# Kernel tuning notes

Measured on AMD Instinct MI355X. Metric: run time of the kernel, lower is better.

Reference implementation:

```python
import jax, jax.numpy as jnp
import numpy as np
from jax import lax

NUM_CLASSES = 8          # channel dim of pred_out -> alphabet of argmax values
NUM_TARGET_LABELS = 8    # fill_max of target_mask -> alphabet of target labels
BIG = 2 ** 30            # sentinel for min-propagation connected components


def connected_components(mask):
    """4-connected components per image. mask: [B,H,W] bool.
    Returns (labels, idx): labels int32, 0 = background; a component's label is
    (min flat index in component) + 1, so labels are unique across the batch.
    Uses min-label propagation to convergence (jit-compatible while_loop)."""
    B, H, W = mask.shape
    idx = jnp.arange(B * H * W, dtype=jnp.int32).reshape(B, H, W) + 1
    lab0 = jnp.where(mask, idx, 0)

    def step(lab):
        l = jnp.where(mask, lab, BIG)
        p = jnp.pad(l, ((0, 0), (1, 1), (1, 1)), constant_values=BIG)
        nb = jnp.minimum(jnp.minimum(p[:, :-2, 1:-1], p[:, 2:, 1:-1]),
                         jnp.minimum(p[:, 1:-1, :-2], p[:, 1:-1, 2:]))
        return jnp.where(mask, jnp.minimum(l, nb), 0)

    def cond(c):
        return jnp.logical_not(c[1])

    def body(c):
        lab, _ = c
        new = step(lab)
        return new, jnp.all(new == lab)

    lab, _ = lax.while_loop(cond, body, (lab0, jnp.array(False)))
    return lab, idx


def bce_dice(pred, target, eps=1e-7, smooth=1.0):
    """BCEDiceLoss: mean binary cross-entropy (pred in [0,1]) + soft dice loss."""
    p = jnp.clip(pred, eps, 1.0 - eps)
    bce = -jnp.mean(target * jnp.log(p) + (1.0 - target) * jnp.log(1.0 - p))
    inter = jnp.sum(pred * target)
    dice = 1.0 - (2.0 * inter + smooth) / (jnp.sum(pred) + jnp.sum(target) + smooth)
    return bce + dice


def build_placeholder(pred_masks):
    """Faithful vectorized form of the per-class / per-component torch loops.
    For each present class v != 0, for each component c != 0 the original does
    placeholder += c_mask * c + last_i  (note: last_i is added GLOBALLY -- we
    replicate that), i.e. placeholder += cc_labels + n_comp * last_i, and
    last_i += len(unique(cc)) = n_comp + (1 if background present)."""
    placeholder = jnp.zeros(pred_masks.shape, dtype=jnp.float32)
    last_i = jnp.int32(1)
    for v in range(1, NUM_CLASSES):  # fixed alphabet of argmax values
        m = pred_masks == v
        present = jnp.any(m)
        lab, idx = connected_components(m)
        n_comp = jnp.sum((lab == idx) & m).astype(jnp.int32)  # one rep per comp
        has_bg = jnp.any(jnp.logical_not(m)).astype(jnp.int32)
        contrib = lab.astype(jnp.float32) + n_comp.astype(jnp.float32) * last_i.astype(jnp.float32)
        placeholder = placeholder + jnp.where(present, contrib, 0.0)
        last_i = last_i + jnp.where(present, n_comp + has_bg, 0)
    return placeholder


def reference(pred_out, target_mask):
    pred_masks = jnp.argmax(pred_out, axis=1)  # [B,H,W]
    # background term
    res = bce_dice((pred_out[:, 0:1] * (pred_masks[:, None] == 0)).astype(jnp.float32),
                   (target_mask == 0).astype(jnp.float32))
    placeholder = build_placeholder(pred_masks)
    # per-target-instance median matching (loop over fixed label alphabet,
    # guarded by presence, since torch loops over the data-dependent unique set)
    for t in range(1, NUM_TARGET_LABELS):
        tm = (target_mask == t)[:, 0]  # [B,H,W]
        n = jnp.sum(tm).astype(jnp.int32)
        present = n > 0
        vals = jnp.sort(jnp.where(tm, placeholder, jnp.inf).ravel())
        med = vals[jnp.maximum(n - 1, 0) // 2]  # torch lower median
        full_med = (placeholder == med).astype(jnp.float32)
        res = res + jnp.where(present, bce_dice(full_med, tm.astype(jnp.float32)), 0.0)
    n_uniq = jnp.sum(jnp.stack([jnp.any(target_mask == t)
                                for t in range(NUM_TARGET_LABELS)])).astype(jnp.float32)
    return res / (n_uniq + 1.0)


def setup_inputs():
    key = jax.random.key(0)
    k1, k2 = jax.random.split(key)
    pred_out = jax.random.uniform(k1, (4, NUM_CLASSES, 512, 512), dtype=jnp.float32)
    target_mask = jax.random.randint(k2, (4, 1, 512, 512), 0, NUM_TARGET_LABELS,
                                     dtype=jnp.int32)
    return {"pred_out": pred_out, "target_mask": target_mask}
```

## Files before the change

kernel.cpp:

```cpp
#include <hip/hip_runtime.h>
#include <math.h>


#define HWMASK (262144 - 1)
#define AL(p) __hip_atomic_load((p), __ATOMIC_RELAXED, __HIP_MEMORY_SCOPE_AGENT)
#define AS(p, v) __hip_atomic_store((p), (v), __ATOMIC_RELAXED, __HIP_MEMORY_SCOPE_AGENT)
#define REL(p, v) __hip_atomic_store((p), (v), __ATOMIC_RELEASE, __HIP_MEMORY_SCOPE_AGENT)
#define ARRIVE(p) __hip_atomic_fetch_add((p), 1u, __ATOMIC_RELAXED, __HIP_MEMORY_SCOPE_AGENT)

static __device__ __forceinline__ int ufind(int* p, int x) {
  while (true) {
    int px = p[x];
    if (px == x) return x;
    int g = p[px];
    if (g == px) return px;
    p[x] = g;
    x = g;
  }
}

static __device__ __forceinline__ int unite(int* p, int a, int b) {
  while (true) {
    a = ufind(p, a); b = ufind(p, b);
    if (a == b) return 0;
    if (a < b) { int old = atomicCAS(&p[b], b, a); if (old == b) return 1; b = old; }
    else       { int old = atomicCAS(&p[a], a, b); if (old == a) return 1; a = old; }
  }
}

__global__ __launch_bounds__(256) void k_argmax(
    const float* __restrict__ pred, const int* __restrict__ tgt,
    int* __restrict__ parent, unsigned char* __restrict__ pk,
    unsigned* __restrict__ stats, unsigned* __restrict__ pcnt,
    double* __restrict__ pdbl, int N) {
  __shared__ unsigned hc[32], ht[32], hA, hB;
  __shared__ double dred[12];
  int tid = threadIdx.x, bid = blockIdx.x;
  if (bid == 0) {
    uint4* z = (uint4*)stats;
    for (int j = tid; j < 6144; j += 256) z[j] = make_uint4(0u, 0u, 0u, 0u);
  }
  if (tid < 32) { hc[tid] = 0; ht[tid] = 0; }
  if (tid == 0) { hA = 0; hB = 0; }
  __syncthreads();
  int wb = (tid >> 6) << 3;
  int n4 = N >> 2, gsz = gridDim.x * blockDim.x;
  double aL = 0.0, aI = 0.0, aP = 0.0;
  unsigned nA = 0, nB = 0;
  for (int i4 = bid * blockDim.x + tid; i4 < n4; i4 += gsz) {
    int i = i4 << 2;
    int b = i >> 18, hw = i & HWMASK;
    const float* pp = pred + ((size_t)b << 21) + hw;
    float4 v[8];
#pragma unroll
    for (int ch = 0; ch < 8; ++ch) v[ch] = *(const float4*)(pp + ((size_t)ch << 18));
    int4 tv = *(const int4*)(tgt + i);
    int tarr[4] = {tv.x & 7, tv.y & 7, tv.z & 7, tv.w & 7};
    unsigned char pkb[4];
#pragma unroll
    for (int j = 0; j < 4; ++j) {
      float p0 = ((const float*)&v[0])[j];
      float best = p0; int c = 0;
#pragma unroll
      for (int ch = 1; ch < 8; ++ch) {
        float x = ((const float*)&v[ch])[j];
        if (x > best) { best = x; c = ch; }
      }
      int t = tarr[j];
      pkb[j] = (unsigned char)(c | (t << 3));
      atomicAdd(&hc[wb + c], 1u);
      atomicAdd(&ht[wb + t], 1u);
      if (c == 0) {
        float pc = fminf(fmaxf(p0, 1e-7f), 1.0f - 1e-7f);
        if (t == 0) { aL += (double)logf(pc); aI += (double)p0; }
        else        { aL += (double)logf(1.0f - pc); }
        aP += (double)p0;
      } else { if (t == 0) nA++; else nB++; }
    }
    *(int4*)(parent + i) = make_int4(i, i + 1, i + 2, i + 3);
    *(uchar4*)(pk + i) = make_uchar4(pkb[0], pkb[1], pkb[2], pkb[3]);
  }
  if (nA) atomicAdd(&hA, nA);
  if (nB) atomicAdd(&hB, nB);
#pragma unroll
  for (int o = 32; o > 0; o >>= 1) {
    aL += __shfl_down(aL, o); aI += __shfl_down(aI, o); aP += __shfl_down(aP, o);
  }
  int wid = tid >> 6, lane = tid & 63;
  if (lane == 0) { dred[wid] = aL; dred[4 + wid] = aI; dred[8 + wid] = aP; }
  __syncthreads();
  if (tid < 8) {
    pcnt[bid * 20 + tid]     = hc[tid] + hc[8 + tid] + hc[16 + tid] + hc[24 + tid];
    pcnt[bid * 20 + 8 + tid] = ht[tid] + ht[8 + tid] + ht[16 + tid] + ht[24 + tid];
  }
  if (tid == 0) {
    pcnt[bid * 20 + 16] = hA; pcnt[bid * 20 + 17] = hB;
    pcnt[bid * 20 + 18] = 0u; pcnt[bid * 20 + 19] = 0u;
    pdbl[bid * 3 + 0] = dred[0] + dred[1] + dred[2] + dred[3];
    pdbl[bid * 3 + 1] = dred[4] + dred[5] + dred[6] + dred[7];
    pdbl[bid * 3 + 2] = dred[8] + dred[9] + dred[10] + dred[11];
  }
}

__global__ __launch_bounds__(256) void k_merge(
    const unsigned char* __restrict__ pk, int* __restrict__ parent,
    unsigned* __restrict__ stats, const unsigned* __restrict__ pcnt,
    unsigned* __restrict__ mcnt, int N, int nbam) {
  __shared__ unsigned lcnt[8], tot[26];
  __shared__ int lastM;
  int tid = threadIdx.x, bid = blockIdx.x;
  if (tid < 8) lcnt[tid] = 0;
  __syncthreads();
  int n4 = N >> 2, gsz = gridDim.x * blockDim.x;
  for (int i4 = bid * blockDim.x + tid; i4 < n4; i4 += gsz) {
    int i = i4 << 2;
    int hw = i & HWMASK;
    uchar4 a = *(const uchar4*)(pk + i);
    unsigned char ca[4] = {(unsigned char)(a.x & 7), (unsigned char)(a.y & 7),
                           (unsigned char)(a.z & 7), (unsigned char)(a.w & 7)};
    if (ca[0] && ca[0] == ca[1] && unite(parent, i,     i + 1)) atomicAdd(&lcnt[ca[0]], 1u);
    if (ca[1] && ca[1] == ca[2] && unite(parent, i + 1, i + 2)) atomicAdd(&lcnt[ca[1]], 1u);
    if (ca[2] && ca[2] == ca[3] && unite(parent, i + 2, i + 3)) atomicAdd(&lcnt[ca[2]], 1u);
    if ((hw & 511) < 508) {
      unsigned char nx = pk[i + 4] & 7;
      if (ca[3] && ca[3] == nx && unite(parent, i + 3, i + 4)) atomicAdd(&lcnt[ca[3]], 1u);
    }
    if ((hw >> 9) < 511) {
      uchar4 d = *(const uchar4*)(pk + i + 512);
      unsigned char da[4] = {(unsigned char)(d.x & 7), (unsigned char)(d.y & 7),
                             (unsigned char)(d.z & 7), (unsigned char)(d.w & 7)};
#pragma unroll
      for (int j = 0; j < 4; ++j)
        if (ca[j] && ca[j] == da[j] && unite(parent, i + j, i + j + 512))
          atomicAdd(&lcnt[ca[j]], 1u);
    }
  }
  __syncthreads();
  if (tid < 8) AS(&mcnt[bid * 8 + tid], lcnt[tid]);
  __syncthreads();
  if (tid == 0) lastM = (ARRIVE(&stats[76]) == gridDim.x - 1) ? 1 : 0;
  __syncthreads();
  if (!lastM) return;
  unsigned S[26];
#pragma unroll
  for (int k = 0; k < 26; ++k) S[k] = 0u;
  for (int b = tid; b < nbam; b += 256) {
    const unsigned* p = pcnt + b * 20;
#pragma unroll
    for (int k = 0; k < 18; ++k) S[k] += p[k];
#pragma unroll
    for (int k = 0; k < 8; ++k) S[18 + k] += AL(&mcnt[b * 8 + k]);
  }
  if (tid < 26) tot[tid] = 0u;
  __syncthreads();
#pragma unroll
  for (int k = 0; k < 26; ++k) {
    unsigned s = S[k];
#pragma unroll
    for (int o = 32; o > 0; o >>= 1) s += __shfl_down(s, o);
    if ((tid & 63) == 0 && s) atomicAdd(&tot[k], s);
  }
  __syncthreads();
  if (tid != 0) return;
  float prodf[8]; int last_i = 1; unsigned pb = 0;
  for (int v = 1; v < 8; ++v) {
    unsigned cntv = tot[v];
    unsigned ncv = cntv - tot[18 + v];
    prodf[v] = 0.0f;
    if (cntv) {
      prodf[v] = __fmul_rn((float)ncv, (float)last_i);
      pb |= 1u << v;
      last_i += (int)ncv + ((cntv < (unsigned)N) ? 1 : 0);
    }
    stats[24 + v] = __float_as_uint(prodf[v]);
  }
  float ph0 = 0.0f;
  for (int v = 1; v < 8; ++v) if (pb & (1u << v)) ph0 = __fadd_rn(ph0, prodf[v]);
  unsigned ab = 0;
  for (int t = 0; t < 8; ++t) stats[8 + t] = tot[8 + t];
  for (int t = 1; t < 8; ++t) {
    unsigned n = tot[8 + t];
    stats[48 + t] = n ? ((n - 1) >> 1) : 0u;
    if (n) ab |= 1u << t;
  }
  stats[32] = pb; stats[33] = ab;
  stats[34] = tot[16]; stats[35] = tot[17];
  unsigned pbits = __float_as_uint(ph0);
  stats[36] = pbits;
  unsigned c;
  if (pbits == 0) c = 64u;
  else {
    int e = (int)(pbits >> 23) - 127;
    int sh = 43 - e;
    if (sh <= 0) c = 64u;
    else if (sh >= 31) c = 0x7FFFFFFFu;
    else c = (1u << sh) + 64u;
  }
  int bl = 32 - __clz((int)c);
  stats[37] = (bl > 8) ? (unsigned)(bl - 8) : 0u;
}

static __device__ void scan_select(unsigned* __restrict__ stats,
                                   const unsigned* __restrict__ ghist,
                                   unsigned abm, int s_cur, unsigned* lh) {
  int tid = threadIdx.x;
  for (int t = 1; t < 8; ++t) {
    if (!(abm >> t & 1u)) continue;
    int k = (int)AL(&stats[48 + t]);
    unsigned cnt = 0;
#pragma unroll
    for (int r = 0; r < 8; ++r)
      cnt += AL(&ghist[r * 2048 + (t << 8) + tid]);
    lh[tid] = cnt;
    __syncthreads();
    for (int o = 1; o < 256; o <<= 1) {
      unsigned v = (tid >= o) ? lh[tid - o] : 0u;
      __syncthreads();
      lh[tid] += v;
      __syncthreads();
    }
    unsigned incl = lh[tid], excl = incl - cnt;
    if ((unsigned)k >= excl && (unsigned)k < incl) {
      atomicOr(&stats[40 + t], ((unsigned)tid) << s_cur);
      AS(&stats[48 + t], (unsigned)(k - (int)excl));
    }
    __syncthreads();
  }
}

static __device__ void finalize_loss(unsigned* __restrict__ stats,
                                     const double* __restrict__ pdbl,
                                     float* __restrict__ out, int N, int nbam,
                                     unsigned ab, double* dred) {
  int tid = threadIdx.x;
  double vL = 0.0, vI = 0.0, vP = 0.0;
  for (int b = tid; b < nbam; b += 256) {
    vL += pdbl[b * 3]; vI += pdbl[b * 3 + 1]; vP += pdbl[b * 3 + 2];
  }
#pragma unroll
  for (int o = 32; o > 0; o >>= 1) {
    vL += __shfl_down(vL, o); vI += __shfl_down(vI, o); vP += __shfl_down(vP, o);
  }
  int wid = tid >> 6, lane = tid & 63;
  if (lane == 0) { dred[wid] = vL; dred[4 + wid] = vI; dred[8 + wid] = vP; }
  __syncthreads();
  if (tid != 0) return;
  vL = dred[0] + dred[1] + dred[2] + dred[3];
  vI = dred[4] + dred[5] + dred[6] + dred[7];
  vP = dred[8] + dred[9] + dred[10] + dred[11];
  double Nd = (double)N;
  const float e32 = 1e-7f;
  const float c1 = 1.0f - e32;
  const float omc1 = 1.0f - c1;
  double lp1 = log((double)c1);
  double lp0 = log((double)e32);
  double l01 = log((double)omc1);
  double l00 = lp1;
  double L = vL + (double)stats[34] * lp0 + (double)stats[35] * l00;
  double res = -L / Nd;
  res += 1.0 - (2.0 * vI + 1.0) / (vP + (double)stats[8] + 1.0);
  for (int t = 1; t < 8; ++t) {
    if (ab >> t & 1u) {
      double a = (double)AL(&stats[56 + t]);
      double f = (double)AL(&stats[64 + t]);
      double n = (double)stats[8 + t];
      double bce = -(a * lp1 + (n - a) * lp0 + (f - a) * l01 + (Nd - n - f + a) * l00) / Nd;
      double dice = 1.0 - (2.0 * a + 1.0) / (f + n + 1.0);
      res += bce + dice;
    }
  }
  int nu = 0;
  for (int t = 0; t < 8; ++t) nu += (stats[8 + t] > 0) ? 1 : 0;
  out[0] = (float)(res / ((double)nu + 1.0));
}

__global__ __launch_bounds__(256, 4) void k_phase2(
    const unsigned char* __restrict__ pk, const int* __restrict__ parent,
    unsigned* __restrict__ stats, unsigned* __restrict__ ghist,
    const double* __restrict__ pdbl, float* __restrict__ out, int N, int nbam) {
  __shared__ unsigned lh[2176];
  __shared__ float sprod[8];
  __shared__ unsigned sw[32];
  __shared__ double dred[12];
  int tid = threadIdx.x;
  int lane = tid & 63;
  if (tid < 8) sprod[tid] = __uint_as_float(stats[24 + tid]);
  if (tid == 0) { sw[0] = stats[32]; sw[1] = stats[33]; sw[2] = stats[36]; sw[3] = stats[37]; }
  for (int j = tid; j < 2176; j += 256) lh[j] = 0u;
  __syncthreads();
  unsigned pb = sw[0], ab = sw[1], ph0 = sw[2];
  int s1 = (int)sw[3];
  unsigned rep = (blockIdx.x & 7) * 2048u;
  int n4 = N >> 2;
  unsigned kk[4];
  unsigned char tv8[4], binv[4];
  int i4 = blockIdx.x * blockDim.x + tid;
  if (i4 < n4) {
    int i = i4 << 2;
    int4 pr = *(const int4*)(parent + i);
    uchar4 pv = *(const uchar4*)(pk + i);
    int parr[4] = {pr.x, pr.y, pr.z, pr.w};
    unsigned char pa[4] = {pv.x, pv.y, pv.z, pv.w};
#pragma unroll
    for (int j = 0; j < 4; ++j) {
      int c = pa[j] & 7, t = pa[j] >> 3;
      float lab = 0.0f;
      if (c) {
        int x = parr[j];
        while (true) { int nx = parent[x]; if (nx == x) break; x = nx; }
        lab = (float)(x + 1);
      }
      float ph = 0.0f;
#pragma unroll
      for (int v = 1; v < 8; ++v) {
        if (pb & (1u << v)) {
          float term = sprod[v];
          if (c == v) term = __fadd_rn(lab, term);
          ph = __fadd_rn(ph, term);
        }
      }
      unsigned kb = __float_as_uint(ph);
      kk[j] = kb; tv8[j] = (unsigned char)t;
      unsigned off = kb - ph0;
      unsigned bin = off >> s1;
      if (bin > 255u) bin = 255u;
      binv[j] = (unsigned char)bin;
    }
  } else {
#pragma unroll
    for (int j = 0; j < 4; ++j) { kk[j] = 0xFFFFFFFFu; tv8[j] = 0; binv[j] = 255; }
  }
#pragma unroll
  for (int e = 0; e < 4; ++e) {
    bool act = (i4 < n4);
    unsigned bin = binv[e];
    int t = tv8[e];
    bool b0 = act && (bin == 0u);
    unsigned long long m0 = __ballot(b0);
    if (b0) {
      if (lane == (int)__ffsll(m0) - 1) atomicAdd(&lh[0], (unsigned)__popcll(m0));
    } else if (act) {
      atomicAdd(&lh[bin], 1u);
    }
#pragma unroll
    for (int tt = 1; tt < 8; ++tt) {
      if (!(ab >> tt & 1u)) continue;
      unsigned long long mt = __ballot(b0 && t == tt);
      if (mt && lane == (int)__ffsll(mt) - 1)
        atomicAdd(&lh[tt * 257], (unsigned)__popcll(mt));
    }
    if (act && bin != 0u && t && (ab >> t & 1u))
      atomicAdd(&lh[t * 257 + bin], 1u);
  }
  __syncthreads();
  for (int j = tid; j < 2048; j += 256) {
    unsigned v = lh[(j >> 8) * 257 + (j & 255)];
    if (v) atomicAdd(&ghist[rep + j], v);
  }
  __syncthreads();
  if (tid == 0) sw[4] = (ARRIVE(&stats[77]) == gridDim.x - 1) ? 1u : 0u;
  __syncthreads();
  if (s1 == 0) {
    if (!sw[4]) return;
    for (int j = tid; j < 2048; j += 256) {
      unsigned s = 0;
#pragma unroll
      for (int r = 0; r < 8; ++r) s += AL(&ghist[r * 2048 + j]);
      lh[j] = s;
    }
    __syncthreads();
    if (tid >= 1 && tid < 8 && (ab >> tid & 1u)) {
      int t = tid;
      unsigned k = stats[48 + t];
      unsigned cum = 0;
      int mb = 255;
      for (int b = 0; b < 256; ++b) {
        unsigned c = lh[(t << 8) + b];
        if (cum + c > k) { mb = b; break; }
        cum += c;
      }
      AS(&stats[56 + t], lh[(t << 8) + mb]);
      AS(&stats[64 + t], lh[mb]);
    }
    __syncthreads();
    finalize_loss(stats, pdbl, out, N, nbam, ab, dred);
    return;
  }
  if (sw[4]) {
    scan_select(stats, ghist, ab, s1, lh);
    for (int j = tid; j < 16384; j += 256) AS(&ghist[j], 0u);
    __syncthreads();
    if (tid == 0) REL(&stats[39], 1u);
  } else {
    if (tid == 0) while (AL(&stats[39]) < 1u) __builtin_amdgcn_s_sleep(2);
    __syncthreads();
  }
  for (int pass = 2; pass <= 4; ++pass) {
    int sprev = s1 - 8 * (pass - 2); if (sprev < 0) sprev = 0;
    int scur  = s1 - 8 * (pass - 1); if (scur  < 0) scur  = 0;
    unsigned maskhi = 0xFFFFFFFFu << sprev;
    if (tid < 8) sw[8 + tid] = AL(&stats[40 + tid]);
    for (int j = tid; j < 2048; j += 256) lh[j] = 0u;
    __syncthreads();
#pragma unroll
    for (int e = 0; e < 4; ++e) {
      int t = tv8[e];
      if (t && (ab >> t & 1u)) {
        unsigned off = kk[e] - ph0;
        if (((off ^ sw[8 + t]) & maskhi) == 0u)
          atomicAdd(&lh[(t << 8) | ((off >> scur) & 255u)], 1u);
      }
    }
    __syncthreads();
    for (int j = tid; j < 2048; j += 256) {
      unsigned v = lh[j];
      if (v) atomicAdd(&ghist[rep + j], v);
    }
    __syncthreads();
    if (tid == 0) sw[5] = (ARRIVE(&stats[76 + pass]) == gridDim.x - 1) ? 1u : 0u;
    __syncthreads();
    if (sw[5]) {
      scan_select(stats, ghist, ab, scur, lh);
      if (scur > 0)
        for (int j = tid; j < 16384; j += 256) AS(&ghist[j], 0u);
      __syncthreads();
      if (tid == 0) REL(&stats[39], (unsigned)pass);
    } else {
      if (tid == 0)
        while (AL(&stats[39]) < (unsigned)pass) __builtin_amdgcn_s_sleep(2);
      __syncthreads();
    }
    if (scur == 0) break;
  }
  if (tid < 16) lh[tid] = 0u;
  if (tid < 8) sw[20 + tid] = ph0 + AL(&stats[40 + tid]);
  __syncthreads();
#pragma unroll
  for (int e = 0; e < 4; ++e) {
    unsigned kb = kk[e];
    int t = tv8[e];
#pragma unroll
    for (int tt = 1; tt < 8; ++tt) {
      if ((ab >> tt & 1u) && kb == sw[20 + tt]) {
        atomicAdd(&lh[8 + tt], 1u);
        if (t == tt) atomicAdd(&lh[tt], 1u);
      }
    }
  }
  __syncthreads();
  if (tid >= 1 && tid < 8) {
    if (lh[8 + tid]) atomicAdd(&stats[64 + tid], lh[8 + tid]);
    if (lh[tid])     atomicAdd(&stats[56 + tid], lh[tid]);
  }
  __syncthreads();
  if (tid == 0) sw[6] = (ARRIVE(&stats[84]) == gridDim.x - 1) ? 1u : 0u;
  __syncthreads();
  if (!sw[6]) return;
  finalize_loss(stats, pdbl, out, N, nbam, ab, dred);
}

extern "C" void kernel_launch(void* const* d_in, const int* in_sizes, int n_in,
                              void* d_out, int out_size, void* d_ws, size_t ws_size,
                              hipStream_t stream) {
  const float* pred = (const float*)d_in[0];
  const int* tgt = (const int*)d_in[1];
  int N = in_sizes[1];
  char* ws = (char*)d_ws;
  int* parent = (int*)ws;
  unsigned char* pk = (unsigned char*)(ws + (size_t)N * 4);
  unsigned* stats = (unsigned*)(ws + (size_t)N * 5);
  unsigned* ghist = stats + 8192;
  unsigned* pcnt = stats + 24576;
  unsigned* mcnt = stats + 45056;
  double* pdbl = (double*)(stats + 53248);
  float* out = (float*)d_out;
  int nbam = 1024;
  int nblk2 = ((N >> 2) + 255) >> 8;

  k_argmax<<<nbam, 256, 0, stream>>>(pred, tgt, parent, pk, stats, pcnt, pdbl, N);
  k_merge<<<nbam, 256, 0, stream>>>(pk, parent, stats, pcnt, mcnt, N, nbam);
  k_phase2<<<nblk2, 256, 0, stream>>>(pk, parent, stats, ghist, pdbl, out, N, nbam);
}
```

Before: 88.97 us.

## Do tile-local union-find in shared memory, merge only tile borders globally

The argmax kernel now gives each block a 16x64 tile and runs union-find on that tile in LDS, then writes tile-root parents to global memory. A separate border-merge kernel unites only pixels across tile edges in global memory, using fewer blocks. The goal is to replace most global atomic union-find traffic and pointer chasing with LDS operations. It adds extra syncthreads and a serial root walk per pixel, and the merge counts are now accumulated from two arrays.

Result: faster. 74.13 us (-16.7%).

```diff
diff --git a/kernel.cpp b/kernel.cpp
--- a/kernel.cpp
+++ b/kernel.cpp
@@ -18,7 +18,6 @@
     x = g;
   }
 }
-
 static __device__ __forceinline__ int unite(int* p, int a, int b) {
   while (true) {
     a = ufind(p, a); b = ufind(p, b);
@@ -27,13 +26,33 @@
     else       { int old = atomicCAS(&p[a], a, b); if (old == a) return 1; a = old; }
   }
 }
-
-__global__ __launch_bounds__(256) void k_argmax(
+static __device__ __forceinline__ int lfind(int* p, int x) {
+  while (true) {
+    int px = p[x];
+    if (px == x) return x;
+    int g = p[px];
+    if (g == px) return px;
+    p[x] = g;
+    x = g;
+  }
+}
+static __device__ __forceinline__ int lunite(int* p, int a, int b) {
+  while (true) {
+    a = lfind(p, a); b = lfind(p, b);
+    if (a == b) return 0;
+    if (a < b) { int old = atomicCAS(&p[b], b, a); if (old == b) return 1; b = old; }
+    else       { int old = atomicCAS(&p[a], a, b); if (old == a) return 1; a = old; }
+  }
+}
+
+__global__ __launch_bounds__(256) void k_argmax_uf(
     const float* __restrict__ pred, const int* __restrict__ tgt,
     int* __restrict__ parent, unsigned char* __restrict__ pk,
     unsigned* __restrict__ stats, unsigned* __restrict__ pcnt,
-    double* __restrict__ pdbl, int N) {
-  __shared__ unsigned hc[32], ht[32], hA, hB;
+    unsigned* __restrict__ mcnt, double* __restrict__ pdbl, int N) {
+  __shared__ int slab[1024];
+  __shared__ unsigned char scls[1024];
+  __shared__ unsigned hc[32], ht[32], lcnt[8], hA, hB;
   __shared__ double dred[12];
   int tid = threadIdx.x, bid = blockIdx.x;
   if (bid == 0) {
@@ -41,45 +60,78 @@
     for (int j = tid; j < 6144; j += 256) z[j] = make_uint4(0u, 0u, 0u, 0u);
   }
   if (tid < 32) { hc[tid] = 0; ht[tid] = 0; }
+  if (tid < 8) lcnt[tid] = 0;
   if (tid == 0) { hA = 0; hB = 0; }
   __syncthreads();
   int wb = (tid >> 6) << 3;
-  int n4 = N >> 2, gsz = gridDim.x * blockDim.x;
+  int img = bid >> 8, trow = (bid & 255) >> 3, tcol = bid & 7;
+  int ly = tid >> 4, lx4 = (tid & 15) << 2;
+  int lj = (ly << 6) + lx4;
+  int gy = (trow << 4) + ly, gx = (tcol << 6) + lx4;
+  int gi = (img << 18) + (gy << 9) + gx;
+  const float* pp = pred + ((size_t)img << 21) + (gy << 9) + gx;
+  float4 v[8];
+#pragma unroll
+  for (int ch = 0; ch < 8; ++ch) v[ch] = *(const float4*)(pp + ((size_t)ch << 18));
+  int4 tv = *(const int4*)(tgt + gi);
+  int tarr[4] = {tv.x & 7, tv.y & 7, tv.z & 7, tv.w & 7};
+  unsigned char pkb[4], carr[4];
   double aL = 0.0, aI = 0.0, aP = 0.0;
   unsigned nA = 0, nB = 0;
-  for (int i4 = bid * blockDim.x + tid; i4 < n4; i4 += gsz) {
-    int i = i4 << 2;
-    int b = i >> 18, hw = i & HWMASK;
-    const float* pp = pred + ((size_t)b << 21) + hw;
-    float4 v[8];
-#pragma unroll
-    for (int ch = 0; ch < 8; ++ch) v[ch] = *(const float4*)(pp + ((size_t)ch << 18));
-    int4 tv = *(const int4*)(tgt + i);
-    int tarr[4] = {tv.x & 7, tv.y & 7, tv.z & 7, tv.w & 7};
-    unsigned char pkb[4];
-#pragma unroll
-    for (int j = 0; j < 4; ++j) {
-      float p0 = ((const float*)&v[0])[j];
-      float best = p0; int c = 0;
-#pragma unroll
-      for (int ch = 1; ch < 8; ++ch) {
-        float x = ((const float*)&v[ch])[j];
-        if (x > best) { best = x; c = ch; }
-      }
-      int t = tarr[j];
-      pkb[j] = (unsigned char)(c | (t << 3));
-      atomicAdd(&hc[wb + c], 1u);
-      atomicAdd(&ht[wb + t], 1u);
-      if (c == 0) {
-        float pc = fminf(fmaxf(p0, 1e-7f), 1.0f - 1e-7f);
-        if (t == 0) { aL += (double)logf(pc); aI += (double)p0; }
-        else        { aL += (double)logf(1.0f - pc); }
-        aP += (double)p0;
-      } else { if (t == 0) nA++; else nB++; }
-    }
-    *(int4*)(parent + i) = make_int4(i, i + 1, i + 2, i + 3);
-    *(uchar4*)(pk + i) = make_uchar4(pkb[0], pkb[1], pkb[2], pkb[3]);
-  }
+#pragma unroll
+  for (int j = 0; j < 4; ++j) {
+    float p0 = ((const float*)&v[0])[j];
+    float best = p0; int c = 0;
+#pragma unroll
+    for (int ch = 1; ch < 8; ++ch) {
+      float x = ((const float*)&v[ch])[j];
+      if (x > best) { best = x; c = ch; }
+    }
+    int t = tarr[j];
+    carr[j] = (unsigned char)c;
+    pkb[j] = (unsigned char)(c | (t << 3));
+    atomicAdd(&hc[wb + c], 1u);
+    atomicAdd(&ht[wb + t], 1u);
+    if (c == 0) {
+      float pc = fminf(fmaxf(p0, 1e-7f), 1.0f - 1e-7f);
+      if (t == 0) { aL += (double)logf(pc); aI += (double)p0; }
+      else        { aL += (double)logf(1.0f - pc); }
+      aP += (double)p0;
+    } else { if (t == 0) nA++; else nB++; }
+  }
+  *(uchar4*)(pk + gi) = make_uchar4(pkb[0], pkb[1], pkb[2], pkb[3]);
+  *(uchar4*)(scls + lj) = make_uchar4(carr[0], carr[1], carr[2], carr[3]);
+  *(int4*)(slab + lj) = make_int4(lj, lj + 1, lj + 2, lj + 3);
+  __syncthreads();
+#pragma unroll
+  for (int k = 0; k < 3; ++k)
+    if (carr[k] && carr[k] == carr[k + 1] && lunite(slab, lj + k, lj + k + 1))
+      atomicAdd(&lcnt[carr[k]], 1u);
+  if (lx4 < 60) {
+    unsigned char nc = scls[lj + 4];
+    if (carr[3] && carr[3] == nc && lunite(slab, lj + 3, lj + 4))
+      atomicAdd(&lcnt[carr[3]], 1u);
+  }
+  if (ly < 15) {
+#pragma unroll
+    for (int k = 0; k < 4; ++k) {
+      unsigned char nc = scls[lj + 64 + k];
+      if (carr[k] && carr[k] == nc && lunite(slab, lj + k, lj + 64 + k))
+        atomicAdd(&lcnt[carr[k]], 1u);
+    }
+  }
+  __syncthreads();
+  int pout[4];
+#pragma unroll
+  for (int k = 0; k < 4; ++k) {
+    pout[k] = gi + k;
+    if (carr[k]) {
+      int r = slab[lj + k];
+      while (true) { int nx = slab[r]; if (nx == r) break; r = nx; }
+      pout[k] = (img << 18) + (((trow << 4) + (r >> 6)) << 9) + (tcol << 6) + (r & 63);
+    }
+  }
+  *(int4*)(parent + gi) = make_int4(pout[0], pout[1], pout[2], pout[3]);
   if (nA) atomicAdd(&hA, nA);
   if (nB) atomicAdd(&hB, nB);
 #pragma unroll
@@ -92,6 +144,7 @@
   if (tid < 8) {
     pcnt[bid * 20 + tid]     = hc[tid] + hc[8 + tid] + hc[16 + tid] + hc[24 + tid];
     pcnt[bid * 20 + 8 + tid] = ht[tid] + ht[8 + tid] + ht[16 + tid] + ht[24 + tid];
+    mcnt[bid * 8 + tid] = lcnt[tid];
   }
   if (tid == 0) {
     pcnt[bid * 20 + 16] = hA; pcnt[bid * 20 + 17] = hB;
@@ -102,41 +155,38 @@
   }
 }
 
-__global__ __launch_bounds__(256) void k_merge(
+__global__ __launch_bounds__(256) void k_bmerge(
     const unsigned char* __restrict__ pk, int* __restrict__ parent,
     unsigned* __restrict__ stats, const unsigned* __restrict__ pcnt,
-    unsigned* __restrict__ mcnt, int N, int nbam) {
+    const unsigned* __restrict__ mcnt, unsigned* __restrict__ bcnt,
+    int N, int nbam) {
   __shared__ unsigned lcnt[8], tot[26];
   __shared__ int lastM;
   int tid = threadIdx.x, bid = blockIdx.x;
   if (tid < 8) lcnt[tid] = 0;
   __syncthreads();
-  int n4 = N >> 2, gsz = gridDim.x * blockDim.x;
-  for (int i4 = bid * blockDim.x + tid; i4 < n4; i4 += gsz) {
-    int i = i4 << 2;
-    int hw = i & HWMASK;
-    uchar4 a = *(const uchar4*)(pk + i);
-    unsigned char ca[4] = {(unsigned char)(a.x & 7), (unsigned char)(a.y & 7),
-                           (unsigned char)(a.z & 7), (unsigned char)(a.w & 7)};
-    if (ca[0] && ca[0] == ca[1] && unite(parent, i,     i + 1)) atomicAdd(&lcnt[ca[0]], 1u);
-    if (ca[1] && ca[1] == ca[2] && unite(parent, i + 1, i + 2)) atomicAdd(&lcnt[ca[1]], 1u);
-    if (ca[2] && ca[2] == ca[3] && unite(parent, i + 2, i + 3)) atomicAdd(&lcnt[ca[2]], 1u);
-    if ((hw & 511) < 508) {
-      unsigned char nx = pk[i + 4] & 7;
-      if (ca[3] && ca[3] == nx && unite(parent, i + 3, i + 4)) atomicAdd(&lcnt[ca[3]], 1u);
-    }
-    if ((hw >> 9) < 511) {
-      uchar4 d = *(const uchar4*)(pk + i + 512);
-      unsigned char da[4] = {(unsigned char)(d.x & 7), (unsigned char)(d.y & 7),
-                             (unsigned char)(d.z & 7), (unsigned char)(d.w & 7)};
-#pragma unroll
-      for (int j = 0; j < 4; ++j)
-        if (ca[j] && ca[j] == da[j] && unite(parent, i + j, i + j + 512))
-          atomicAdd(&lcnt[ca[j]], 1u);
-    }
-  }
-  __syncthreads();
-  if (tid < 8) AS(&mcnt[bid * 8 + tid], lcnt[tid]);
+  int B = N >> 18;
+  int Eh = B * 3584;
+  int E = Eh + B * 15872;
+  int gsz = gridDim.x * blockDim.x;
+  for (int e = bid * blockDim.x + tid; e < E; e += gsz) {
+    int gi1, gi2;
+    if (e < Eh) {
+      int img = e / 3584, rem = e % 3584;
+      int x = ((rem >> 9) << 6) + 63, y = rem & 511;
+      gi1 = (img << 18) + (y << 9) + x; gi2 = gi1 + 1;
+    } else {
+      int e2 = e - Eh;
+      int img = e2 / 15872, rem = e2 % 15872;
+      int y = ((rem >> 9) << 4) + 15, x = rem & 511;
+      gi1 = (img << 18) + (y << 9) + x; gi2 = gi1 + 512;
+    }
+    int c1 = pk[gi1] & 7;
+    if (c1 && c1 == (pk[gi2] & 7) && unite(parent, gi1, gi2))
+      atomicAdd(&lcnt[c1], 1u);
+  }
+  __syncthreads();
+  if (tid < 8) AS(&bcnt[bid * 8 + tid], lcnt[tid]);
   __syncthreads();
   if (tid == 0) lastM = (ARRIVE(&stats[76]) == gridDim.x - 1) ? 1 : 0;
   __syncthreads();
@@ -149,8 +199,11 @@
 #pragma unroll
     for (int k = 0; k < 18; ++k) S[k] += p[k];
 #pragma unroll
-    for (int k = 0; k < 8; ++k) S[18 + k] += AL(&mcnt[b * 8 + k]);
-  }
+    for (int k = 0; k < 8; ++k) S[18 + k] += mcnt[b * 8 + k];
+  }
+  for (int b = tid; b < (int)gridDim.x; b += 256)
+#pragma unroll
+    for (int k = 0; k < 8; ++k) S[18 + k] += AL(&bcnt[b * 8 + k]);
   if (tid < 26) tot[tid] = 0u;
   __syncthreads();
 #pragma unroll
@@ -473,11 +526,12 @@
   unsigned* pcnt = stats + 24576;
   unsigned* mcnt = stats + 45056;
   double* pdbl = (double*)(stats + 53248);
+  unsigned* bcnt = stats + 59392;
   float* out = (float*)d_out;
-  int nbam = 1024;
+  int nbam = N >> 10;
   int nblk2 = ((N >> 2) + 255) >> 8;
 
-  k_argmax<<<nbam, 256, 0, stream>>>(pred, tgt, parent, pk, stats, pcnt, pdbl, N);
-  k_merge<<<nbam, 256, 0, stream>>>(pk, parent, stats, pcnt, mcnt, N, nbam);
+  k_argmax_uf<<<nbam, 256, 0, stream>>>(pred, tgt, parent, pk, stats, pcnt, mcnt, pdbl, N);
+  k_bmerge<<<256, 256, 0, stream>>>(pk, parent, stats, pcnt, mcnt, bcnt, N, nbam);
   k_phase2<<<nblk2, 256, 0, stream>>>(pk, parent, stats, ghist, pdbl, out, N, nbam);
 }
```
